# Performance work log

Hardware: AMD Instinct MI355X
Metric: run time of the kernel (lower is better)

## Reference

```python
import jax, jax.numpy as jnp
import numpy as np

EMB = 1024
HID = 4096
B = 2
T = 4096
NUM_BLOCK = 24
EPS = 1e-6


def rmsnorm(x):
    # unparameterized RMS normalization over last dim
    return x * jax.lax.rsqrt(jnp.mean(jnp.square(x), axis=-1, keepdims=True) + EPS)


def setup_inputs() -> dict:
    key = jax.random.key(0)
    k1, k2, k3, k4 = jax.random.split(key, 4)
    x = jax.random.normal(k1, (B, T, EMB), dtype=jnp.float32)
    W1 = 0.02 * jax.random.normal(k2, (HID, EMB), dtype=jnp.float32)
    W2 = 0.02 * jax.random.normal(k3, (HID, EMB), dtype=jnp.float32)
    W3 = (0.02 / np.sqrt(NUM_BLOCK)) * jax.random.normal(k4, (EMB, HID), dtype=jnp.float32)
    return {"x": x, "W1": W1, "W2": W2, "W3": W3}


def bar_quadratic_causal_preact_stable(a, b):
    # y_t = (1/t^2) * sum_{i<=t} sum_{j<=t} exp(a_i + b_j), per feature channel.
    # exp factorizes, so compute stably via log-cumsum-exp along the seq axis.
    seq = a.shape[1]
    log_t = jnp.log(jnp.arange(1, seq + 1, dtype=a.dtype))  # [T]
    la = jax.lax.cumlogsumexp(a, axis=1)  # [B,T,H]
    lb = jax.lax.cumlogsumexp(b, axis=1)  # [B,T,H]
    return jnp.exp(la + lb - 2.0 * log_t[None, :, None])


def reference(x, W1, W2, W3):
    r = rmsnorm(x)
    a = jnp.einsum('bte,he->bth', r, W1)  # fc_1, no bias
    b = jnp.einsum('bte,he->bth', r, W2)  # fc_2, no bias
    r = bar_quadratic_causal_preact_stable(a, b)
    r = rmsnorm(r)
    r = jnp.einsum('bth,eh->bte', r, W3)  # fc_3, no bias
    return x + r
```

## Files before the change

kernel.cpp:

```cpp
#include <hip/hip_runtime.h>
#include <hip/hip_fp8.h>

#define EMB 1024
#define HID 4096
#define NB 2
#define TT 4096
#define MROWS (NB*TT)
#define N1 (2*HID)
#define CHUNK 128
#define NCH 32

typedef short short8 __attribute__((ext_vector_type(8)));
typedef float v4f   __attribute__((ext_vector_type(4)));

__device__ __forceinline__ unsigned short f2bf(float f) {
  unsigned int u = __float_as_uint(f);
  u += 0x7FFFu + ((u >> 16) & 1u);
  return (unsigned short)(u >> 16);
}
__device__ __forceinline__ float bf2f(unsigned short s) {
  return __uint_as_float(((unsigned int)s) << 16);
}
__device__ __forceinline__ float h2f(unsigned short u) {
  return (float)(*(const _Float16*)&u);
}
__device__ __forceinline__ unsigned char f2e4m3(float f) {
  __hip_fp8_e4m3 q(f);
  return *(unsigned char*)&q;
}
__device__ __forceinline__ float e4m32f(unsigned char c) {
  __hip_fp8_e4m3 q = *(__hip_fp8_e4m3*)&c;
  return (float)q;
}
__device__ __forceinline__ void g2l16(const void* g, void* l) {
  __builtin_amdgcn_global_load_lds(
      (const __attribute__((address_space(1))) void*)g,
      (__attribute__((address_space(3))) void*)l, 16, 0, 0);
}

__device__ __forceinline__ float block_reduce_sum(float v, float* sbuf) {
  #pragma unroll
  for (int off = 32; off; off >>= 1) v += __shfl_down(v, off, 64);
  int lane = threadIdx.x & 63, w = threadIdx.x >> 6;
  if (lane == 0) sbuf[w] = v;
  __syncthreads();
  return sbuf[0] + sbuf[1] + sbuf[2] + sbuf[3];
}

__global__ __launch_bounds__(256) void conv_all(const float* __restrict__ W1,
                                                const float* __restrict__ W2,
                                                const float* __restrict__ W3,
                                                unsigned short* __restrict__ o12,
                                                unsigned short* __restrict__ o3) {
  size_t i = ((size_t)blockIdx.x*256 + threadIdx.x)*4;
  const float* s; unsigned short* d;
  if (i < (size_t)HID*EMB)        { s = W1 + i;                      d = o12 + i; }
  else if (i < 2ull*HID*EMB)      { s = W2 + (i - (size_t)HID*EMB);  d = o12 + i; }
  else                            { s = W3 + (i - 2ull*HID*EMB);     d = o3 + (i - 2ull*HID*EMB); }
  float4 v = *(const float4*)s;
  ushort4 u; u.x=f2bf(v.x); u.y=f2bf(v.y); u.z=f2bf(v.z); u.w=f2bf(v.w);
  *(ushort4*)d = u;
}

__global__ __launch_bounds__(256) void rmsnorm_x(const float* __restrict__ x,
                                                 unsigned short* __restrict__ r) {
  __shared__ float sbuf[4];
  int row = blockIdx.x;
  float4 v = *(const float4*)(x + (size_t)row*EMB + threadIdx.x*4);
  float ss = v.x*v.x + v.y*v.y + v.z*v.z + v.w*v.w;
  float tot = block_reduce_sum(ss, sbuf);
  float sc = rsqrtf(tot * (1.0f/EMB) + 1e-6f);
  ushort4 o; o.x=f2bf(v.x*sc); o.y=f2bf(v.y*sc); o.z=f2bf(v.z*sc); o.w=f2bf(v.w*sc);
  *(ushort4*)(r + (size_t)row*EMB + threadIdx.x*4) = o;
}

__global__ __launch_bounds__(256) void rowssq(const unsigned short* __restrict__ y,
                                              float* __restrict__ sc) {
  __shared__ float sbuf[4];
  int row = blockIdx.x;
  const unsigned short* p = y + (size_t)row*HID + threadIdx.x*16;
  short8 v0 = *(const short8*)p;
  short8 v1 = *(const short8*)(p+8);
  float ss = 0.f;
  #pragma unroll
  for (int j=0;j<8;++j){ float a=bf2f((unsigned short)v0[j]), b=bf2f((unsigned short)v1[j]); ss += a*a + b*b; }
  float tot = block_reduce_sum(ss, sbuf);
  if (threadIdx.x == 0) sc[row] = rsqrtf(tot*(1.0f/HID) + 1e-6f);
}

__global__ __launch_bounds__(256, 2)
void gemm_exp(const unsigned short* __restrict__ A,
              const unsigned short* __restrict__ Bt,
              unsigned char* __restrict__ C8,
              float* __restrict__ part,
              int K, int N) {
  __shared__ short lA[128*64];
  __shared__ short lB[128*64];
  const int tid  = threadIdx.x;
  const int lane = tid & 63;
  const int wm   = (tid >> 6) >> 1, wn = (tid >> 6) & 1;
  const int rowBase = blockIdx.y * 128;
  const int colBase = blockIdx.x * 128;

  v4f acc[4][4];
  #pragma unroll
  for (int i=0;i<4;++i)
    #pragma unroll
    for (int j=0;j<4;++j) acc[i][j] = (v4f){0.f,0.f,0.f,0.f};

  for (int k0 = 0; k0 < K; k0 += 64) {
    #pragma unroll
    for (int j = 0; j < 4; ++j) {
      int s = j*256 + tid;
      int m = s >> 3;
      int c = (s & 7) ^ (m & 7);
      g2l16(A + (size_t)(rowBase + m)*K + k0 + c*8, &lA[s*8]);
    }
    #pragma unroll
    for (int j = 0; j < 4; ++j) {
      int s = j*256 + tid;
      int m = s >> 3;
      int c = (s & 7) ^ (m & 7);
      g2l16(Bt + (size_t)(colBase + m)*K + k0 + c*8, &lB[s*8]);
    }
    __syncthreads();
    #pragma unroll
    for (int s2 = 0; s2 < 2; ++s2) {
      const int quad = lane >> 4;
      const int cc = s2*4 + quad;
      short8 aF[4], bF[4];
      #pragma unroll
      for (int mt = 0; mt < 4; ++mt) {
        int ml = wm*64 + mt*16 + (lane & 15);
        aF[mt] = *(const short8*)&lA[(ml*8 + (cc ^ (ml & 7)))*8];
      }
      #pragma unroll
      for (int nt = 0; nt < 4; ++nt) {
        int nl = wn*64 + nt*16 + (lane & 15);
        bF[nt] = *(const short8*)&lB[(nl*8 + (cc ^ (nl & 7)))*8];
      }
      #pragma unroll
      for (int mt = 0; mt < 4; ++mt)
        #pragma unroll
        for (int nt = 0; nt < 4; ++nt)
          acc[mt][nt] = __builtin_amdgcn_mfma_f32_16x16x32_bf16(aF[mt], bF[nt], acc[mt][nt], 0, 0, 0);
    }
    __syncthreads();
  }

  const int quad = lane >> 4, c15 = lane & 15;
  float csum[4] = {0.f, 0.f, 0.f, 0.f};
  #pragma unroll
  for (int mt = 0; mt < 4; ++mt) {
    #pragma unroll
    for (int nt = 0; nt < 4; ++nt) {
      int col = colBase + wn*64 + nt*16 + c15;
      #pragma unroll
      for (int r = 0; r < 4; ++r) {
        int row = rowBase + wm*64 + mt*16 + quad*4 + r;
        size_t idx = (size_t)row*N + col;
        float e = __expf(acc[mt][nt][r]);
        C8[idx] = f2e4m3(e);
        csum[nt] += e;
      }
    }
  }
  float* cs = (float*)lA;
  #pragma unroll
  for (int nt = 0; nt < 4; ++nt) {
    float s = csum[nt];
    s += __shfl_xor(s, 16, 64);
    s += __shfl_xor(s, 32, 64);
    if (lane < 16) cs[wm*128 + wn*64 + nt*16 + lane] = s;
  }
  __syncthreads();
  if (tid < 128)
    part[(size_t)(colBase + tid)*64 + blockIdx.y] = cs[tid] + cs[128 + tid];
}

__global__ __launch_bounds__(256, 2)
void gemm_out(const unsigned short* __restrict__ A,
              const unsigned short* __restrict__ Bt,
              unsigned short* __restrict__ Ph,
              int K, int KCH, int N) {
  __shared__ short lA[128*64];
  __shared__ short lB[128*64];
  const int tid  = threadIdx.x;
  const int lane = tid & 63;
  const int wm   = (tid >> 6) >> 1, wn = (tid >> 6) & 1;
  const int rowBase = blockIdx.y * 128;
  const int colBase = blockIdx.x * 128;
  const int kStart  = blockIdx.z * KCH;

  v4f acc[4][4];
  #pragma unroll
  for (int i=0;i<4;++i)
    #pragma unroll
    for (int j=0;j<4;++j) acc[i][j] = (v4f){0.f,0.f,0.f,0.f};

  for (int k0 = kStart; k0 < kStart + KCH; k0 += 64) {
    #pragma unroll
    for (int j = 0; j < 4; ++j) {
      int s = j*256 + tid;
      int m = s >> 3;
      int c = (s & 7) ^ (m & 7);
      g2l16(A + (size_t)(rowBase + m)*K + k0 + c*8, &lA[s*8]);
    }
    #pragma unroll
    for (int j = 0; j < 4; ++j) {
      int s = j*256 + tid;
      int m = s >> 3;
      int c = (s & 7) ^ (m & 7);
      g2l16(Bt + (size_t)(colBase + m)*K + k0 + c*8, &lB[s*8]);
    }
    __syncthreads();
    #pragma unroll
    for (int s2 = 0; s2 < 2; ++s2) {
      const int quad = lane >> 4;
      const int cc = s2*4 + quad;
      short8 aF[4], bF[4];
      #pragma unroll
      for (int mt = 0; mt < 4; ++mt) {
        int ml = wm*64 + mt*16 + (lane & 15);
        aF[mt] = *(const short8*)&lA[(ml*8 + (cc ^ (ml & 7)))*8];
      }
      #pragma unroll
      for (int nt = 0; nt < 4; ++nt) {
        int nl = wn*64 + nt*16 + (lane & 15);
        bF[nt] = *(const short8*)&lB[(nl*8 + (cc ^ (nl & 7)))*8];
      }
      #pragma unroll
      for (int mt = 0; mt < 4; ++mt)
        #pragma unroll
        for (int nt = 0; nt < 4; ++nt)
          acc[mt][nt] = __builtin_amdgcn_mfma_f32_16x16x32_bf16(aF[mt], bF[nt], acc[mt][nt], 0, 0, 0);
    }
    __syncthreads();
  }

  const int quad = lane >> 4, c15 = lane & 15;
  #pragma unroll
  for (int mt = 0; mt < 4; ++mt) {
    #pragma unroll
    for (int nt = 0; nt < 4; ++nt) {
      int col = colBase + wn*64 + nt*16 + c15;
      #pragma unroll
      for (int r = 0; r < 4; ++r) {
        int row = rowBase + wm*64 + mt*16 + quad*4 + r;
        size_t idx = ((size_t)blockIdx.z*MROWS + row)*N + col;
        _Float16 h = (_Float16)acc[mt][nt][r];
        Ph[idx] = *(unsigned short*)&h;
      }
    }
  }
}

__global__ __launch_bounds__(256) void scan_prefix(float* __restrict__ part) {
  int idx = blockIdx.x*256 + threadIdx.x;
  int col = idx >> 1, bb = idx & 1;
  float* p = part + (size_t)col*64 + bb*NCH;
  float run = 0.f;
  #pragma unroll
  for (int c = 0; c < NCH; ++c) { float v = p[c]; p[c] = run; run += v; }
}

__global__ __launch_bounds__(256) void scan_emit(const unsigned char* __restrict__ ab,
                                                 const float* __restrict__ part,
                                                 unsigned short* __restrict__ y) {
  int h = blockIdx.x*256 + threadIdx.x;
  int cy = blockIdx.y, bb = blockIdx.z;
  float sa = part[(size_t)h*64 + bb*NCH + cy];
  float sb = part[(size_t)(HID + h)*64 + bb*NCH + cy];
  const unsigned char* pa = ab + ((size_t)(bb*TT + cy*CHUNK))*N1 + h;
  const unsigned char* pb = pa + HID;
  unsigned short* py = y + ((size_t)(bb*TT + cy*CHUNK))*HID + h;
  int t0 = cy*CHUNK;
  #pragma unroll 4
  for (int i = 0; i < CHUNK; ++i) {
    sa += e4m32f(pa[(size_t)i*N1]);
    sb += e4m32f(pb[(size_t)i*N1]);
    float inv = 1.0f / (float)(t0 + i + 1);
    py[(size_t)i*HID] = f2bf(sa*sb*inv*inv);
  }
}

__global__ __launch_bounds__(256) void reduce_out(const unsigned short* __restrict__ p,
                                                  const float* __restrict__ x,
                                                  const float* __restrict__ Sc,
                                                  float* __restrict__ o) {
  size_t i = ((size_t)blockIdx.x*256 + threadIdx.x)*4;
  int row = (int)(i >> 10);
  float4 xv = *(const float4*)(x + i);
  float s0 = 0.f, s1 = 0.f, s2 = 0.f, s3 = 0.f;
  #pragma unroll
  for (int z = 0; z < 4; ++z) {
    ushort4 u = *(const ushort4*)(p + (size_t)z*MROWS*EMB + i);
    s0 += h2f(u.x); s1 += h2f(u.y); s2 += h2f(u.z); s3 += h2f(u.w);
  }
  float sc = Sc[row];
  float4 ov; ov.x = xv.x + sc*s0; ov.y = xv.y + sc*s1; ov.z = xv.z + sc*s2; ov.w = xv.w + sc*s3;
  *(float4*)(o + i) = ov;
}

extern "C" void kernel_launch(void* const* d_in, const int* in_sizes, int n_in,
                              void* d_out, int out_size, void* d_ws, size_t ws_size,
                              hipStream_t stream) {
  const float* x  = (const float*)d_in[0];
  const float* W1 = (const float*)d_in[1];
  const float* W2 = (const float*)d_in[2];
  const float* W3 = (const float*)d_in[3];
  float* out = (float*)d_out;
  char* ws = (char*)d_ws;

  unsigned short* r_bf   = (unsigned short*)(ws);
  unsigned short* w12_bf = (unsigned short*)(ws + 16777216ull);
  unsigned short* w3_bf  = (unsigned short*)(ws + 33554432ull);
  unsigned char*  ab8    = (unsigned char*) (ws + 41943040ull);
  unsigned short* y_bf   = (unsigned short*)(ws + 109051904ull);
  float*          sc     = (float*)(ws + 176160768ull);
  unsigned short* psum   = (unsigned short*)ab8;
  float*          part   = (float*)d_out;

  conv_all<<<12288, 256, 0, stream>>>(W1, W2, W3, w12_bf, w3_bf);
  rmsnorm_x<<<MROWS, 256, 0, stream>>>(x, r_bf);
  gemm_exp<<<dim3(64,64), 256, 0, stream>>>(r_bf, w12_bf, ab8, part, EMB, N1);
  scan_prefix<<<64, 256, 0, stream>>>(part);
  scan_emit<<<dim3(16,NCH,2), 256, 0, stream>>>(ab8, part, y_bf);
  rowssq<<<MROWS, 256, 0, stream>>>(y_bf, sc);
  gemm_out<<<dim3(8,64,4), 256, 0, stream>>>(y_bf, w3_bf, psum, HID, 1024, EMB);
  reduce_out<<<8192, 256, 0, stream>>>(psum, x, sc, out);
}
```

Before: 407.1 us.

## Run the output GEMM in FP8 with pre-normalized, quantized activations and weights

W3 is now quantized to e4m3 with a fixed scale of 64. The row-norm pass now applies the RMS scale and writes FP8 activations, where before it only produced per-row scales. gemm_out uses the fp8 16x16x32 MFMA over 128-wide K tiles, which halves operand bytes and LDS traffic per K step. The final reduce applies a constant 1/64 rescale in place of per-row scales. This trades accuracy in the output projection for lower memory and compute cost.

```diff
diff --git a/kernel.cpp b/kernel.cpp
--- a/kernel.cpp
+++ b/kernel.cpp
@@ -51,15 +51,20 @@
                                                 const float* __restrict__ W2,
                                                 const float* __restrict__ W3,
                                                 unsigned short* __restrict__ o12,
-                                                unsigned short* __restrict__ o3) {
+                                                unsigned char* __restrict__ o3) {
   size_t i = ((size_t)blockIdx.x*256 + threadIdx.x)*4;
-  const float* s; unsigned short* d;
-  if (i < (size_t)HID*EMB)        { s = W1 + i;                      d = o12 + i; }
-  else if (i < 2ull*HID*EMB)      { s = W2 + (i - (size_t)HID*EMB);  d = o12 + i; }
-  else                            { s = W3 + (i - 2ull*HID*EMB);     d = o3 + (i - 2ull*HID*EMB); }
-  float4 v = *(const float4*)s;
-  ushort4 u; u.x=f2bf(v.x); u.y=f2bf(v.y); u.z=f2bf(v.z); u.w=f2bf(v.w);
-  *(ushort4*)d = u;
+  if (i < 2ull*HID*EMB) {
+    const float* s = (i < (size_t)HID*EMB) ? (W1 + i) : (W2 + (i - (size_t)HID*EMB));
+    float4 v = *(const float4*)s;
+    ushort4 u; u.x=f2bf(v.x); u.y=f2bf(v.y); u.z=f2bf(v.z); u.w=f2bf(v.w);
+    *(ushort4*)(o12 + i) = u;
+  } else {
+    size_t off = i - 2ull*HID*EMB;
+    float4 v = *(const float4*)(W3 + off);
+    uchar4 u; u.x=f2e4m3(v.x*64.f); u.y=f2e4m3(v.y*64.f);
+             u.z=f2e4m3(v.z*64.f); u.w=f2e4m3(v.w*64.f);
+    *(uchar4*)(o3 + off) = u;
+  }
 }
 
 __global__ __launch_bounds__(256) void rmsnorm_x(const float* __restrict__ x,
@@ -74,18 +79,31 @@
   *(ushort4*)(r + (size_t)row*EMB + threadIdx.x*4) = o;
 }
 
-__global__ __launch_bounds__(256) void rowssq(const unsigned short* __restrict__ y,
-                                              float* __restrict__ sc) {
+__global__ __launch_bounds__(256) void normq(const unsigned short* __restrict__ y,
+                                             unsigned char* __restrict__ y8) {
   __shared__ float sbuf[4];
   int row = blockIdx.x;
   const unsigned short* p = y + (size_t)row*HID + threadIdx.x*16;
   short8 v0 = *(const short8*)p;
   short8 v1 = *(const short8*)(p+8);
-  float ss = 0.f;
-  #pragma unroll
-  for (int j=0;j<8;++j){ float a=bf2f((unsigned short)v0[j]), b=bf2f((unsigned short)v1[j]); ss += a*a + b*b; }
+  float f[16]; float ss = 0.f;
+  #pragma unroll
+  for (int j=0;j<8;++j){ f[j]=bf2f((unsigned short)v0[j]); f[j+8]=bf2f((unsigned short)v1[j]); }
+  #pragma unroll
+  for (int j=0;j<16;++j) ss += f[j]*f[j];
   float tot = block_reduce_sum(ss, sbuf);
-  if (threadIdx.x == 0) sc[row] = rsqrtf(tot*(1.0f/HID) + 1e-6f);
+  float sc = rsqrtf(tot*(1.0f/HID) + 1e-6f);
+  unsigned int w[4];
+  #pragma unroll
+  for (int g=0; g<4; ++g) {
+    unsigned int a0 = f2e4m3(f[g*4+0]*sc);
+    unsigned int a1 = f2e4m3(f[g*4+1]*sc);
+    unsigned int a2 = f2e4m3(f[g*4+2]*sc);
+    unsigned int a3 = f2e4m3(f[g*4+3]*sc);
+    w[g] = a0 | (a1<<8) | (a2<<16) | (a3<<24);
+  }
+  uint4 o; o.x=w[0]; o.y=w[1]; o.z=w[2]; o.w=w[3];
+  *(uint4*)(y8 + (size_t)row*HID + threadIdx.x*16) = o;
 }
 
 __global__ __launch_bounds__(256, 2)
@@ -179,12 +197,12 @@
 }
 
 __global__ __launch_bounds__(256, 2)
-void gemm_out(const unsigned short* __restrict__ A,
-              const unsigned short* __restrict__ Bt,
+void gemm_out(const unsigned char* __restrict__ A8,
+              const unsigned char* __restrict__ B8,
               unsigned short* __restrict__ Ph,
               int K, int KCH, int N) {
-  __shared__ short lA[128*64];
-  __shared__ short lB[128*64];
+  __shared__ unsigned char lA8[128*128];
+  __shared__ unsigned char lB8[128*128];
   const int tid  = threadIdx.x;
   const int lane = tid & 63;
   const int wm   = (tid >> 6) >> 1, wn = (tid >> 6) & 1;
@@ -198,42 +216,43 @@
     #pragma unroll
     for (int j=0;j<4;++j) acc[i][j] = (v4f){0.f,0.f,0.f,0.f};
 
-  for (int k0 = kStart; k0 < kStart + KCH; k0 += 64) {
+  for (int k0 = kStart; k0 < kStart + KCH; k0 += 128) {
     #pragma unroll
     for (int j = 0; j < 4; ++j) {
       int s = j*256 + tid;
       int m = s >> 3;
       int c = (s & 7) ^ (m & 7);
-      g2l16(A + (size_t)(rowBase + m)*K + k0 + c*8, &lA[s*8]);
+      g2l16(A8 + (size_t)(rowBase + m)*K + k0 + c*16, &lA8[s*16]);
     }
     #pragma unroll
     for (int j = 0; j < 4; ++j) {
       int s = j*256 + tid;
       int m = s >> 3;
       int c = (s & 7) ^ (m & 7);
-      g2l16(Bt + (size_t)(colBase + m)*K + k0 + c*8, &lB[s*8]);
+      g2l16(B8 + (size_t)(colBase + m)*K + k0 + c*16, &lB8[s*16]);
     }
     __syncthreads();
     #pragma unroll
-    for (int s2 = 0; s2 < 2; ++s2) {
+    for (int s2 = 0; s2 < 4; ++s2) {
       const int quad = lane >> 4;
-      const int cc = s2*4 + quad;
-      short8 aF[4], bF[4];
+      const int cc = s2*2 + (quad >> 1);
+      const int hh = quad & 1;
+      long aF[4], bF[4];
       #pragma unroll
       for (int mt = 0; mt < 4; ++mt) {
         int ml = wm*64 + mt*16 + (lane & 15);
-        aF[mt] = *(const short8*)&lA[(ml*8 + (cc ^ (ml & 7)))*8];
+        aF[mt] = *(const long*)&lA8[ml*128 + ((cc ^ (ml & 7))<<4) + (hh<<3)];
       }
       #pragma unroll
       for (int nt = 0; nt < 4; ++nt) {
         int nl = wn*64 + nt*16 + (lane & 15);
-        bF[nt] = *(const short8*)&lB[(nl*8 + (cc ^ (nl & 7)))*8];
+        bF[nt] = *(const long*)&lB8[nl*128 + ((cc ^ (nl & 7))<<4) + (hh<<3)];
       }
       #pragma unroll
       for (int mt = 0; mt < 4; ++mt)
         #pragma unroll
         for (int nt = 0; nt < 4; ++nt)
-          acc[mt][nt] = __builtin_amdgcn_mfma_f32_16x16x32_bf16(aF[mt], bF[nt], acc[mt][nt], 0, 0, 0);
+          acc[mt][nt] = __builtin_amdgcn_mfma_f32_16x16x32_fp8_fp8(aF[mt], bF[nt], acc[mt][nt], 0, 0, 0);
     }
     __syncthreads();
   }
@@ -286,10 +305,8 @@
 
 __global__ __launch_bounds__(256) void reduce_out(const unsigned short* __restrict__ p,
                                                   const float* __restrict__ x,
-                                                  const float* __restrict__ Sc,
                                                   float* __restrict__ o) {
   size_t i = ((size_t)blockIdx.x*256 + threadIdx.x)*4;
-  int row = (int)(i >> 10);
   float4 xv = *(const float4*)(x + i);
   float s0 = 0.f, s1 = 0.f, s2 = 0.f, s3 = 0.f;
   #pragma unroll
@@ -297,8 +314,9 @@
     ushort4 u = *(const ushort4*)(p + (size_t)z*MROWS*EMB + i);
     s0 += h2f(u.x); s1 += h2f(u.y); s2 += h2f(u.z); s3 += h2f(u.w);
   }
-  float sc = Sc[row];
-  float4 ov; ov.x = xv.x + sc*s0; ov.y = xv.y + sc*s1; ov.z = xv.z + sc*s2; ov.w = xv.w + sc*s3;
+  const float inv64 = 1.0f/64.0f;
+  float4 ov; ov.x = xv.x + inv64*s0; ov.y = xv.y + inv64*s1;
+             ov.z = xv.z + inv64*s2; ov.w = xv.w + inv64*s3;
   *(float4*)(o + i) = ov;
 }
 
@@ -314,19 +332,19 @@
 
   unsigned short* r_bf   = (unsigned short*)(ws);
   unsigned short* w12_bf = (unsigned short*)(ws + 16777216ull);
-  unsigned short* w3_bf  = (unsigned short*)(ws + 33554432ull);
-  unsigned char*  ab8    = (unsigned char*) (ws + 41943040ull);
-  unsigned short* y_bf   = (unsigned short*)(ws + 109051904ull);
-  float*          sc     = (float*)(ws + 176160768ull);
+  unsigned char*  w3_8   = (unsigned char*) (ws + 33554432ull);
+  unsigned char*  ab8    = (unsigned char*) (ws + 37748736ull);
+  unsigned short* y_bf   = (unsigned short*)(ws + 104857600ull);
+  unsigned char*  y8     = (unsigned char*) (ws + 171966464ull);
   unsigned short* psum   = (unsigned short*)ab8;
   float*          part   = (float*)d_out;
 
-  conv_all<<<12288, 256, 0, stream>>>(W1, W2, W3, w12_bf, w3_bf);
+  conv_all<<<12288, 256, 0, stream>>>(W1, W2, W3, w12_bf, w3_8);
   rmsnorm_x<<<MROWS, 256, 0, stream>>>(x, r_bf);
   gemm_exp<<<dim3(64,64), 256, 0, stream>>>(r_bf, w12_bf, ab8, part, EMB, N1);
   scan_prefix<<<64, 256, 0, stream>>>(part);
   scan_emit<<<dim3(16,NCH,2), 256, 0, stream>>>(ab8, part, y_bf);
-  rowssq<<<MROWS, 256, 0, stream>>>(y_bf, sc);
-  gemm_out<<<dim3(8,64,4), 256, 0, stream>>>(y_bf, w3_bf, psum, HID, 1024, EMB);
-  reduce_out<<<8192, 256, 0, stream>>>(psum, x, sc, out);
-}
+  normq<<<MROWS, 256, 0, stream>>>(y_bf, y8);
+  gemm_out<<<dim3(8,64,4), 256, 0, stream>>>(y8, w3_8, psum, HID, 1024, EMB);
+  reduce_out<<<8192, 256, 0, stream>>>(psum, x, out);
+}
```

Result: faster. 389.7 us (-4.3%).
